# Performance work log

Measured on AMD Instinct MI355X. Metric: run time of the kernel, lower is better.

Reference implementation:

```python
import jax, jax.numpy as jnp
import numpy as np

B, T, C = 4, 1024, 1024
H, HKV, D = 16, 4, 64
GATE_CH = 12
ROPE_THETA = 10000.0


def _rms_norm(x):
    # F.rms_norm with default eps = machine epsilon of dtype, no learnable scale
    eps = jnp.finfo(x.dtype).eps
    ms = jnp.mean(jnp.square(x), axis=-1, keepdims=True)
    return x * jax.lax.rsqrt(ms + eps)


def _apply_rotary(x, cos, sin):
    # x: (B, T, h, D); cos/sin: (1, T, 1, D//2). Half-split rotation.
    d = x.shape[-1] // 2
    x1, x2 = x[..., :d], x[..., d:]
    y1 = x1 * cos + x2 * sin
    y2 = -x1 * sin + x2 * cos
    return jnp.concatenate([y1, y2], axis=-1)


def setup_inputs() -> dict:
    key = jax.random.key(0)
    ks = jax.random.split(key, 8)
    x = jax.random.normal(ks[0], (B, T, C), dtype=jnp.float32)
    ve = jax.random.normal(ks[1], (B, T, HKV * D), dtype=jnp.float32)
    # real RoPE tables, shape (1, T, 1, D//2)
    half = D // 2
    inv_freq = 1.0 / (ROPE_THETA ** (np.arange(half, dtype=np.float32) / half))
    freqs = np.arange(T, dtype=np.float32)[:, None] * inv_freq[None, :]
    cos = jnp.asarray(np.cos(freqs), dtype=jnp.float32).reshape(1, T, 1, half)
    sin = jnp.asarray(np.sin(freqs), dtype=jnp.float32).reshape(1, T, 1, half)
    s = 0.02
    Wq = jax.random.normal(ks[2], (H * D, C), dtype=jnp.float32) * s
    Wk = jax.random.normal(ks[3], (HKV * D, C), dtype=jnp.float32) * s
    Wv = jax.random.normal(ks[4], (HKV * D, C), dtype=jnp.float32) * s
    Wo = jax.random.normal(ks[5], (C, C), dtype=jnp.float32) * s
    Wg = jax.random.normal(ks[6], (HKV, GATE_CH), dtype=jnp.float32) * s
    return {"x": x, "ve": ve, "cos": cos, "sin": sin,
            "Wq": Wq, "Wk": Wk, "Wv": Wv, "Wo": Wo, "Wg": Wg,
            "window_size": 256}


def reference(x, ve, cos, sin, Wq, Wk, Wv, Wo, Wg, window_size):
    b, t, c = x.shape
    d = 2 * cos.shape[-1]
    h = Wq.shape[0] // d
    hkv = Wk.shape[0] // d
    rep = h // hkv

    q = (x @ Wq.T).reshape(b, t, h, d)
    k = (x @ Wk.T).reshape(b, t, hkv, d)
    v = (x @ Wv.T).reshape(b, t, hkv, d)

    # value-embedding sigmoid gate (3 * sigmoid of first 12 channels of x)
    gate = 3.0 * jax.nn.sigmoid(x[..., : Wg.shape[1]] @ Wg.T)  # (b, t, hkv)
    v = v + gate[..., None] * ve.reshape(b, t, hkv, d)

    q = _apply_rotary(q, cos, sin)
    k = _apply_rotary(k, cos, sin)
    q = _rms_norm(q) * 1.2
    k = _rms_norm(k) * 1.2

    # GQA attention with sliding-window causal mask (left=window_size, right=0)
    qg = q.reshape(b, t, hkv, rep, d)
    scale = 1.0 / jnp.sqrt(jnp.asarray(d, dtype=q.dtype))
    scores = jnp.einsum('bqgrd,bkgd->bgrqk', qg, k) * scale
    i = jnp.arange(t)[:, None]
    j = jnp.arange(t)[None, :]
    mask = (j <= i) & ((i - j) <= window_size)  # (t, t)
    scores = jnp.where(mask[None, None, None], scores, -jnp.inf)
    probs = jax.nn.softmax(scores, axis=-1)
    y = jnp.einsum('bgrqk,bkgd->bqgrd', probs, v).reshape(b, t, h * d)
    return y @ Wo.T
```

## Files before the change

### kernel.cpp

```cpp
#include <hip/hip_runtime.h>

typedef __bf16 v8bf __attribute__((ext_vector_type(8)));
typedef float v4f __attribute__((ext_vector_type(4)));
typedef unsigned int v4u __attribute__((ext_vector_type(4)));
typedef unsigned int v2u __attribute__((ext_vector_type(2)));
typedef unsigned short u16;

#define DEVI static __device__ __forceinline__

DEVI float bf2f(u16 u) {
    union { float f; unsigned int i; } c; c.i = ((unsigned int)u) << 16; return c.f;
}
DEVI u16 f2bf(float f) {
    union { __bf16 b; u16 u; } c; c.b = (__bf16)f;
    return c.u;
}

union Frag { v4u u; v8bf v; u16 h[8]; };

#define GLD16(gptr, lptr) __builtin_amdgcn_global_load_lds( \
    (const __attribute__((address_space(1))) void*)(gptr),  \
    (__attribute__((address_space(3))) void*)(lptr), 16, 0, 0)

__global__ __launch_bounds__(256) void convert6(
    const float* __restrict__ x, const float* __restrict__ wq,
    const float* __restrict__ wk, const float* __restrict__ wv,
    const float* __restrict__ wo, const float* __restrict__ Wg,
    u16* __restrict__ xb, u16* __restrict__ wb, u16* __restrict__ wob,
    float* __restrict__ gates)
{
    if (blockIdx.y == 5) {
        const int stride = gridDim.x * 256;
        for (int i = blockIdx.x * 256 + threadIdx.x; i < 4096 * 4; i += stride) {
            const int token = i >> 2, g = i & 3;
            float dot = 0.f;
#pragma unroll
            for (int c = 0; c < 12; c++)
                dot += x[token * 1024 + c] * Wg[g * 12 + c];
            gates[i] = 3.f / (1.f + __expf(-dot));
        }
        return;
    }
    const float* src; u16* dst; int n;
    switch (blockIdx.y) {
        case 0: src = x;  dst = xb;               n = 4096 * 1024; break;
        case 1: src = wq; dst = wb;               n = 1024 * 1024; break;
        case 2: src = wk; dst = wb + 1024 * 1024; n = 256 * 1024;  break;
        case 3: src = wv; dst = wb + 1280 * 1024; n = 256 * 1024;  break;
        default: src = wo; dst = wob;             n = 1024 * 1024; break;
    }
    const int stride = gridDim.x * 256 * 4;
    for (int i = (blockIdx.x * 256 + threadIdx.x) * 4; i < n; i += stride) {
        const float4 f = *(const float4*)(src + i);
        v2u p;
        p[0] = (unsigned int)f2bf(f.x) | ((unsigned int)f2bf(f.y) << 16);
        p[1] = (unsigned int)f2bf(f.z) | ((unsigned int)f2bf(f.w) << 16);
        *(v2u*)(dst + i) = p;
    }
}

template <bool QKV>
__global__ __launch_bounds__(256) void gemm_bt(
    const u16* __restrict__ A, const u16* __restrict__ B,
    void* __restrict__ Cv, int N,
    const float* __restrict__ cs, const float* __restrict__ sn,
    const float* __restrict__ gates, const float* __restrict__ ve,
    u16* __restrict__ qn, u16* __restrict__ kn, u16* __restrict__ vn)
{
    __shared__ __align__(16) u16 As[64 * 64];
    __shared__ __align__(16) u16 Bs[128 * 64];
    const int tid  = threadIdx.x;
    const int lane = tid & 63, l15 = lane & 15, quad = (lane >> 4) & 3;
    const int w    = tid >> 6;
    const int wr   = (w >> 1) * 32, wc = (w & 1) * 64;
    const int m0   = blockIdx.x * 64, n0 = blockIdx.y * 128;

    const u16* ab = A + m0 * 1024;
    const u16* bb = B + n0 * 1024;
    const int r0 = tid >> 3;
    const int c0 = (tid & 7) * 8;
    const u16* ag = ab + r0 * 1024 + c0;
    const u16* bg = bb + r0 * 1024 + c0;
    u16* al = &As[r0 * 64 + c0];
    u16* bl = &Bs[r0 * 64 + c0];

    v4f acc[2][4];
    const v4f vzero = {0.f, 0.f, 0.f, 0.f};
#pragma unroll
    for (int i = 0; i < 2; i++)
#pragma unroll
        for (int j = 0; j < 4; j++) acc[i][j] = vzero;

    for (int k0 = 0; k0 < 1024; k0 += 64) {
        __syncthreads();
        GLD16(ag + k0,             al);
        GLD16(ag + k0 + 32 * 1024, al + 32 * 64);
        GLD16(bg + k0,             bl);
        GLD16(bg + k0 + 32 * 1024, bl + 32 * 64);
        GLD16(bg + k0 + 64 * 1024, bl + 64 * 64);
        GLD16(bg + k0 + 96 * 1024, bl + 96 * 64);
        __syncthreads();
#pragma unroll
        for (int ks = 0; ks < 2; ks++) {
            v8bf af[2];
#pragma unroll
            for (int mi = 0; mi < 2; mi++)
                af[mi] = *(const v8bf*)&As[(wr + mi * 16 + l15) * 64 + ks * 32 + quad * 8];
#pragma unroll
            for (int ni = 0; ni < 4; ni++) {
                v8bf bv = *(const v8bf*)&Bs[(wc + ni * 16 + l15) * 64 + ks * 32 + quad * 8];
#pragma unroll
                for (int mi = 0; mi < 2; mi++)
                    acc[mi][ni] = __builtin_amdgcn_mfma_f32_16x16x32_bf16(af[mi], bv, acc[mi][ni], 0, 0, 0);
            }
        }
    }

    if (!QKV) {
#pragma unroll
        for (int mi = 0; mi < 2; mi++) {
            const int row = m0 + wr + mi * 16 + quad * 4;
#pragma unroll
            for (int ni = 0; ni < 4; ni++) {
                const int col = n0 + wc + ni * 16 + l15;
#pragma unroll
                for (int r = 0; r < 4; r++)
                    ((float*)Cv)[(row + r) * N + col] = acc[mi][ni][r];
            }
        }
        return;
    }

    const int hcol = n0 + wc;
    if (hcol < 1280) {
        const bool isQ = (hcol < 1024);
        u16* dst = isQ ? (qn + (hcol >> 6) * 64) : (kn + ((hcol - 1024) >> 6) * 64);
        const int dstride = isQ ? 1024 : 256;
#pragma unroll
        for (int mi = 0; mi < 2; mi++) {
#pragma unroll
            for (int r = 0; r < 4; r++) {
                const int row = m0 + wr + mi * 16 + quad * 4 + r;
                const int pos = row & 1023;
                const float c0 = cs[pos * 32 + l15],      s0 = sn[pos * 32 + l15];
                const float c1 = cs[pos * 32 + 16 + l15], s1 = sn[pos * 32 + 16 + l15];
                const float y0 = acc[mi][0][r] * c0 + acc[mi][2][r] * s0;
                const float y2 = acc[mi][2][r] * c0 - acc[mi][0][r] * s0;
                const float y1 = acc[mi][1][r] * c1 + acc[mi][3][r] * s1;
                const float y3 = acc[mi][3][r] * c1 - acc[mi][1][r] * s1;
                float ss = y0 * y0 + y1 * y1 + y2 * y2 + y3 * y3;
#pragma unroll
                for (int off = 8; off >= 1; off >>= 1)
                    ss += __shfl_xor(ss, off, 64);
                const float inv = rsqrtf(ss * (1.0f / 64.0f) + 1.1920929e-7f) * 1.2f;
                u16* d = dst + row * dstride;
                d[l15]      = f2bf(y0 * inv);
                d[16 + l15] = f2bf(y1 * inv);
                d[32 + l15] = f2bf(y2 * inv);
                d[48 + l15] = f2bf(y3 * inv);
            }
        }
    } else {
        const int g = (hcol - 1280) >> 6;
#pragma unroll
        for (int mi = 0; mi < 2; mi++) {
#pragma unroll
            for (int r = 0; r < 4; r++) {
                const int row = m0 + wr + mi * 16 + quad * 4 + r;
                const float gate = gates[row * 4 + g];
                u16* d = vn + row * 256 + g * 64;
                const float* vesrc = ve + row * 256 + g * 64;
#pragma unroll
                for (int ni = 0; ni < 4; ni++)
                    d[ni * 16 + l15] = f2bf(acc[mi][ni][r] + gate * vesrc[ni * 16 + l15]);
            }
        }
    }
}

__global__ __launch_bounds__(256) void vtrans(
    const u16* __restrict__ vn, u16* __restrict__ vt)
{
    __shared__ __align__(16) u16 T[64 * 72];
    const int tid = threadIdx.x;
    const int t0  = blockIdx.x * 64, g = blockIdx.y, b = blockIdx.z;
    {
        const int row = tid >> 2, ch = (tid & 3) * 16;
        const int goff = (b * 1024 + t0 + row) * 256 + g * 64 + ch;
        *(v4u*)&T[row * 72 + ch]     = *(const v4u*)&vn[goff];
        *(v4u*)&T[row * 72 + ch + 8] = *(const v4u*)&vn[goff + 8];
    }
    __syncthreads();
    {
        const int d = tid >> 2, tc = (tid & 3) * 16;
        Frag o0, o1;
#pragma unroll
        for (int j = 0; j < 8; j++) {
            o0.h[j] = T[(tc + j) * 72 + d];
            o1.h[j] = T[(tc + 8 + j) * 72 + d];
        }
        u16* dst = vt + ((b * 4 + g) * 64 + d) * 1024 + t0 + tc;
        *(v4u*)dst       = o0.u;
        *(v4u*)(dst + 8) = o1.u;
    }
}

__global__ __launch_bounds__(256) void attn(
    const u16* __restrict__ qn, const u16* __restrict__ kn,
    const u16* __restrict__ vt, u16* __restrict__ yo)
{
    __shared__ __align__(16) u16 Ks[64 * 72];
    __shared__ __align__(16) u16 VTs[64 * 72];
    __shared__ __align__(16) u16 Ps[4][32 * 72];
    const int tid  = threadIdx.x;
    const int w    = tid >> 6, lane = tid & 63, l15 = lane & 15, quad = (lane >> 4) & 3;
    const int qb   = blockIdx.x, h = blockIdx.y, b = blockIdx.z;
    const int g    = h >> 2;
    const int qbase = qb * 128;
    const int qabs0 = qbase + w * 32;
    const int tok0  = b * 1024 + qabs0;
    u16* pw = Ps[w];

    v8bf qf[2][2];
#pragma unroll
    for (int mi = 0; mi < 2; mi++)
#pragma unroll
        for (int ks = 0; ks < 2; ks++) {
            Frag f;
            f.u = *(const v4u*)&qn[(tok0 + mi * 16 + l15) * 1024 + h * 64 + ks * 32 + quad * 8];
#pragma unroll
            for (int j = 0; j < 8; j++) f.h[j] = f2bf(0.18033688f * bf2f(f.h[j]));
            qf[mi][ks] = f.v;
        }

    v4f o[2][4];
    float li[2][4];
    const v4f vzero = {0.f, 0.f, 0.f, 0.f};
#pragma unroll
    for (int mi = 0; mi < 2; mi++) {
#pragma unroll
        for (int nd = 0; nd < 4; nd++) o[mi][nd] = vzero;
#pragma unroll
        for (int r = 0; r < 4; r++) li[mi][r] = 0.f;
    }

    const int kstart = (qbase >= 256) ? qbase - 256 : 0;
    const int kend   = qbase + 64;
    for (int kbase = kstart; kbase <= kend; kbase += 64) {
        __syncthreads();
        {
            const int row = tid >> 2, ch = (tid & 3) * 16;
            const int goff = (b * 1024 + kbase + row) * 256 + g * 64 + ch;
            *(v4u*)&Ks[row * 72 + ch]     = *(const v4u*)&kn[goff];
            *(v4u*)&Ks[row * 72 + ch + 8] = *(const v4u*)&kn[goff + 8];
            const u16* vsrc = vt + ((b * 4 + g) * 64 + row) * 1024 + kbase + ch;
            *(v4u*)&VTs[row * 72 + ch]     = *(const v4u*)vsrc;
            *(v4u*)&VTs[row * 72 + ch + 8] = *(const v4u*)(vsrc + 8);
        }
        __syncthreads();

        bool skip2[2][4], full2[2][4];
#pragma unroll
        for (int mi = 0; mi < 2; mi++)
#pragma unroll
            for (int ni = 0; ni < 4; ni++) {
                const int qw = qabs0 + mi * 16;
                const int left = kbase + ni * 16;
                skip2[mi][ni] = (left > qw + 15) || (qw - (left + 15) > 256);
                full2[mi][ni] = ((left + 15) <= qw) && ((qw + 15 - left) <= 256);
            }

#pragma unroll
        for (int mi = 0; mi < 2; mi++) {
#pragma unroll
            for (int ni = 0; ni < 4; ni++) {
                if (skip2[mi][ni]) {
#pragma unroll
                    for (int r = 0; r < 4; r++)
                        pw[(mi * 16 + quad * 4 + r) * 72 + ni * 16 + l15] = 0;
                    continue;
                }
                v8bf kf0 = *(const v8bf*)&Ks[(ni * 16 + l15) * 72 + quad * 8];
                v8bf kf1 = *(const v8bf*)&Ks[(ni * 16 + l15) * 72 + 32 + quad * 8];
                v4f a = vzero;
                a = __builtin_amdgcn_mfma_f32_16x16x32_bf16(qf[mi][0], kf0, a, 0, 0, 0);
                a = __builtin_amdgcn_mfma_f32_16x16x32_bf16(qf[mi][1], kf1, a, 0, 0, 0);
                if (!full2[mi][ni]) {
                    const int kj = kbase + ni * 16 + l15;
#pragma unroll
                    for (int r = 0; r < 4; r++) {
                        const int qi = qabs0 + mi * 16 + quad * 4 + r;
                        if (!((kj <= qi) && (qi - kj <= 256))) a[r] = -1e30f;
                    }
                }
#pragma unroll
                for (int r = 0; r < 4; r++) {
                    const float p = exp2f(a[r] - 17.312340f);
                    li[mi][r] += p;
                    pw[(mi * 16 + quad * 4 + r) * 72 + ni * 16 + l15] = f2bf(p);
                }
            }
        }

#pragma unroll
        for (int mi = 0; mi < 2; mi++)
#pragma unroll
            for (int ks = 0; ks < 2; ks++) {
                if (skip2[mi][2 * ks] && skip2[mi][2 * ks + 1]) continue;
                v8bf af = *(const v8bf*)&pw[(mi * 16 + l15) * 72 + ks * 32 + quad * 8];
#pragma unroll
                for (int nd = 0; nd < 4; nd++) {
                    v8bf bv = *(const v8bf*)&VTs[(nd * 16 + l15) * 72 + ks * 32 + quad * 8];
                    o[mi][nd] = __builtin_amdgcn_mfma_f32_16x16x32_bf16(af, bv, o[mi][nd], 0, 0, 0);
                }
            }
    }

#pragma unroll
    for (int mi = 0; mi < 2; mi++) {
#pragma unroll
        for (int off = 8; off >= 1; off >>= 1)
#pragma unroll
            for (int r = 0; r < 4; r++)
                li[mi][r] += __shfl_xor(li[mi][r], off, 64);
        float inv[4];
#pragma unroll
        for (int r = 0; r < 4; r++) inv[r] = 1.f / li[mi][r];
#pragma unroll
        for (int nd = 0; nd < 4; nd++) {
            const int col = h * 64 + nd * 16 + l15;
#pragma unroll
            for (int r = 0; r < 4; r++) {
                const int row = tok0 + mi * 16 + quad * 4 + r;
                yo[row * 1024 + col] = f2bf(o[mi][nd][r] * inv[r]);
            }
        }
    }
}

extern "C" void kernel_launch(void* const* d_in, const int* in_sizes, int n_in,
                              void* d_out, int out_size, void* d_ws, size_t ws_size,
                              hipStream_t stream)
{
    const float* x  = (const float*)d_in[0];
    const float* ve = (const float*)d_in[1];
    const float* cs = (const float*)d_in[2];
    const float* sn = (const float*)d_in[3];
    const float* Wq = (const float*)d_in[4];
    const float* Wk = (const float*)d_in[5];
    const float* Wv = (const float*)d_in[6];
    const float* Wo = (const float*)d_in[7];
    const float* Wg = (const float*)d_in[8];

    u16*   xb    = (u16*)d_ws;
    u16*   wb    = xb  + 4096 * 1024;
    u16*   wob   = wb  + 1536 * 1024;
    u16*   qn    = wob + 1024 * 1024;
    u16*   kn    = qn  + 4096 * 1024;
    u16*   vn    = kn  + 4096 * 256;
    u16*   vt    = vn  + 4096 * 256;
    u16*   ay    = vt  + 4096 * 256;
    float* gates = (float*)(ay + 4096 * 1024);

    convert6<<<dim3(512, 6), 256, 0, stream>>>(x, Wq, Wk, Wv, Wo, Wg, xb, wb, wob, gates);
    gemm_bt<true><<<dim3(64, 12), 256, 0, stream>>>(xb, wb, nullptr, 1536,
                                                    cs, sn, gates, ve, qn, kn, vn);
    vtrans<<<dim3(16, 4, 4), 256, 0, stream>>>(vn, vt);
    attn<<<dim3(8, 16, 4), 256, 0, stream>>>(qn, kn, vt, ay);
    gemm_bt<false><<<dim3(64, 8), 256, 0, stream>>>(ay, wob, d_out, 1024,
                                                    nullptr, nullptr, nullptr, nullptr,
                                                    nullptr, nullptr, nullptr);
}
```

Baseline: 160.7 us.

## Fuse V transpose into QKV GEMM epilogue and hoist K fragment loads

The V-projection blocks of the QKV GEMM now stage the gated V tile in shared memory, reusing the GEMM's tile buffer, and write it out already transposed. This removes the separate vtrans kernel launch and the global round trip through the intermediate vn buffer. The attention inner loop is reordered so each K fragment is loaded from LDS once per key column block and shared across both query sub-tiles, and columns fully masked for both sub-tiles are skipped as a whole. The cost is extra block-wide barriers in the V epilogue and strided LDS reads during the transpose.

```diff
diff --git a/kernel.cpp b/kernel.cpp
--- a/kernel.cpp
+++ b/kernel.cpp
@@ -65,10 +65,11 @@
     void* __restrict__ Cv, int N,
     const float* __restrict__ cs, const float* __restrict__ sn,
     const float* __restrict__ gates, const float* __restrict__ ve,
-    u16* __restrict__ qn, u16* __restrict__ kn, u16* __restrict__ vn)
+    u16* __restrict__ qn, u16* __restrict__ kn, u16* __restrict__ vt)
 {
-    __shared__ __align__(16) u16 As[64 * 64];
-    __shared__ __align__(16) u16 Bs[128 * 64];
+    __shared__ __align__(16) u16 smem[12288];
+    u16* As = smem;
+    u16* Bs = smem + 4096;
     const int tid  = threadIdx.x;
     const int lane = tid & 63, l15 = lane & 15, quad = (lane >> 4) & 3;
     const int w    = tid >> 6;
@@ -142,12 +143,12 @@
             for (int r = 0; r < 4; r++) {
                 const int row = m0 + wr + mi * 16 + quad * 4 + r;
                 const int pos = row & 1023;
-                const float c0 = cs[pos * 32 + l15],      s0 = sn[pos * 32 + l15];
-                const float c1 = cs[pos * 32 + 16 + l15], s1 = sn[pos * 32 + 16 + l15];
-                const float y0 = acc[mi][0][r] * c0 + acc[mi][2][r] * s0;
-                const float y2 = acc[mi][2][r] * c0 - acc[mi][0][r] * s0;
-                const float y1 = acc[mi][1][r] * c1 + acc[mi][3][r] * s1;
-                const float y3 = acc[mi][3][r] * c1 - acc[mi][1][r] * s1;
+                const float c0_ = cs[pos * 32 + l15],      s0_ = sn[pos * 32 + l15];
+                const float c1_ = cs[pos * 32 + 16 + l15], s1_ = sn[pos * 32 + 16 + l15];
+                const float y0 = acc[mi][0][r] * c0_ + acc[mi][2][r] * s0_;
+                const float y2 = acc[mi][2][r] * c0_ - acc[mi][0][r] * s0_;
+                const float y1 = acc[mi][1][r] * c1_ + acc[mi][3][r] * s1_;
+                const float y3 = acc[mi][3][r] * c1_ - acc[mi][1][r] * s1_;
                 float ss = y0 * y0 + y1 * y1 + y2 * y2 + y3 * y3;
 #pragma unroll
                 for (int off = 8; off >= 1; off >>= 1)
@@ -161,47 +162,42 @@
             }
         }
     } else {
-        const int g = (hcol - 1280) >> 6;
+        const int g  = (hcol - 1280) >> 6;
+        const int hb = wc >> 6;
+        u16* vbuf = smem;
+        __syncthreads();
 #pragma unroll
         for (int mi = 0; mi < 2; mi++) {
 #pragma unroll
             for (int r = 0; r < 4; r++) {
-                const int row = m0 + wr + mi * 16 + quad * 4 + r;
+                const int tl  = wr + mi * 16 + quad * 4 + r;
+                const int row = m0 + tl;
                 const float gate = gates[row * 4 + g];
-                u16* d = vn + row * 256 + g * 64;
                 const float* vesrc = ve + row * 256 + g * 64;
 #pragma unroll
                 for (int ni = 0; ni < 4; ni++)
-                    d[ni * 16 + l15] = f2bf(acc[mi][ni][r] + gate * vesrc[ni * 16 + l15]);
-            }
-        }
-    }
-}
-
-__global__ __launch_bounds__(256) void vtrans(
-    const u16* __restrict__ vn, u16* __restrict__ vt)
-{
-    __shared__ __align__(16) u16 T[64 * 72];
-    const int tid = threadIdx.x;
-    const int t0  = blockIdx.x * 64, g = blockIdx.y, b = blockIdx.z;
-    {
-        const int row = tid >> 2, ch = (tid & 3) * 16;
-        const int goff = (b * 1024 + t0 + row) * 256 + g * 64 + ch;
-        *(v4u*)&T[row * 72 + ch]     = *(const v4u*)&vn[goff];
-        *(v4u*)&T[row * 72 + ch + 8] = *(const v4u*)&vn[goff + 8];
-    }
-    __syncthreads();
-    {
-        const int d = tid >> 2, tc = (tid & 3) * 16;
-        Frag o0, o1;
-#pragma unroll
-        for (int j = 0; j < 8; j++) {
-            o0.h[j] = T[(tc + j) * 72 + d];
-            o1.h[j] = T[(tc + 8 + j) * 72 + d];
-        }
-        u16* dst = vt + ((b * 4 + g) * 64 + d) * 1024 + t0 + tc;
-        *(v4u*)dst       = o0.u;
-        *(v4u*)(dst + 8) = o1.u;
+                    vbuf[hb * 4608 + tl * 72 + ni * 16 + l15] =
+                        f2bf(acc[mi][ni][r] + gate * vesrc[ni * 16 + l15]);
+            }
+        }
+        __syncthreads();
+        {
+            const int rowi = tid >> 1;
+            const int hb2 = rowi >> 6, d = rowi & 63;
+            const int gg = ((n0 - 1280) >> 6) + hb2;
+            const int bB = m0 >> 10, t0 = m0 & 1023;
+            const int half = (tid & 1) * 32;
+            Frag f[4];
+#pragma unroll
+            for (int ck = 0; ck < 4; ck++)
+#pragma unroll
+                for (int j = 0; j < 8; j++)
+                    f[ck].h[j] = vbuf[hb2 * 4608 + (half + ck * 8 + j) * 72 + d];
+            u16* dst = vt + ((bB * 4 + gg) * 64 + d) * 1024 + t0 + half;
+#pragma unroll
+            for (int ck = 0; ck < 4; ck++)
+                *(v4u*)(dst + ck * 8) = f[ck].u;
+        }
     }
 }
 
@@ -271,17 +267,25 @@
             }
 
 #pragma unroll
-        for (int mi = 0; mi < 2; mi++) {
-#pragma unroll
-            for (int ni = 0; ni < 4; ni++) {
+        for (int ni = 0; ni < 4; ni++) {
+            if (skip2[0][ni] && skip2[1][ni]) {
+#pragma unroll
+                for (int mi = 0; mi < 2; mi++)
+#pragma unroll
+                    for (int r = 0; r < 4; r++)
+                        pw[(mi * 16 + quad * 4 + r) * 72 + ni * 16 + l15] = 0;
+                continue;
+            }
+            v8bf kf0 = *(const v8bf*)&Ks[(ni * 16 + l15) * 72 + quad * 8];
+            v8bf kf1 = *(const v8bf*)&Ks[(ni * 16 + l15) * 72 + 32 + quad * 8];
+#pragma unroll
+            for (int mi = 0; mi < 2; mi++) {
                 if (skip2[mi][ni]) {
 #pragma unroll
                     for (int r = 0; r < 4; r++)
                         pw[(mi * 16 + quad * 4 + r) * 72 + ni * 16 + l15] = 0;
                     continue;
                 }
-                v8bf kf0 = *(const v8bf*)&Ks[(ni * 16 + l15) * 72 + quad * 8];
-                v8bf kf1 = *(const v8bf*)&Ks[(ni * 16 + l15) * 72 + 32 + quad * 8];
                 v4f a = vzero;
                 a = __builtin_amdgcn_mfma_f32_16x16x32_bf16(qf[mi][0], kf0, a, 0, 0, 0);
                 a = __builtin_amdgcn_mfma_f32_16x16x32_bf16(qf[mi][1], kf1, a, 0, 0, 0);
@@ -357,15 +361,13 @@
     u16*   wob   = wb  + 1536 * 1024;
     u16*   qn    = wob + 1024 * 1024;
     u16*   kn    = qn  + 4096 * 1024;
-    u16*   vn    = kn  + 4096 * 256;
-    u16*   vt    = vn  + 4096 * 256;
+    u16*   vt    = kn  + 4096 * 256;
     u16*   ay    = vt  + 4096 * 256;
     float* gates = (float*)(ay + 4096 * 1024);
 
     convert6<<<dim3(512, 6), 256, 0, stream>>>(x, Wq, Wk, Wv, Wo, Wg, xb, wb, wob, gates);
     gemm_bt<true><<<dim3(64, 12), 256, 0, stream>>>(xb, wb, nullptr, 1536,
-                                                    cs, sn, gates, ve, qn, kn, vn);
-    vtrans<<<dim3(16, 4, 4), 256, 0, stream>>>(vn, vt);
+                                                    cs, sn, gates, ve, qn, kn, vt);
     attn<<<dim3(8, 16, 4), 256, 0, stream>>>(qn, kn, vt, ay);
     gemm_bt<false><<<dim3(64, 8), 256, 0, stream>>>(ay, wob, d_out, 1024,
                                                     nullptr, nullptr, nullptr, nullptr,
```

New measurement: 161.2 us. No clear change (+0.3%).
